# Kernel optimization log

Measured on AMD Instinct MI355X. Metric: run time of the kernel, lower is better.

## Reference

```python
import jax, jax.numpy as jnp
import numpy as np

B, S, D = 4, 4096, 1024
ROT = 4          # rotation_dim (quaternion)
MAX_SEQ = 4096   # max_seq_len
EPS = 1e-5


def setup_inputs() -> dict:
    key = jax.random.key(0)
    k_x, = jax.random.split(key, 1)
    x = jax.random.normal(k_x, (B, S, D), dtype=jnp.float32)
    # Learned parameters (torch inits: eye, ones, LN gamma=1 beta=0)
    rotation_matrix = jnp.eye(ROT, dtype=jnp.float32)
    frequency_kernel = jnp.ones((MAX_SEQ,), dtype=jnp.float32)
    ln_gamma = jnp.ones((D,), dtype=jnp.float32)
    ln_beta = jnp.zeros((D,), dtype=jnp.float32)
    return {"x": x, "rotation_matrix": rotation_matrix,
            "frequency_kernel": frequency_kernel,
            "ln_gamma": ln_gamma, "ln_beta": ln_beta}


def reference(x, rotation_matrix, frequency_kernel, ln_gamma, ln_beta):
    b, s, d = x.shape
    quat_dim = d // ROT
    # (b, s, quat_dim, 4)
    x_quat = x.reshape(b, s, quat_dim, ROT)
    # FFT along sequence axis, multiply by (real) learnable frequency kernel
    x_freq = jnp.fft.fft(x_quat, axis=1)
    kernel = frequency_kernel[:s].reshape(1, s, 1, 1)
    filtered_time = jnp.fft.ifft(x_freq * kernel, axis=1).real.astype(x.dtype)
    # Small 4x4 quaternion rotation applied to the last axis
    rotated = jnp.einsum('bstq,oq->bsto', filtered_time, rotation_matrix)
    out = rotated.reshape(b, s, d)
    # LayerNorm over the feature dim
    mean = jnp.mean(out, axis=-1, keepdims=True)
    var = jnp.var(out, axis=-1, keepdims=True)
    out = (out - mean) * jax.lax.rsqrt(var + EPS) * ln_gamma + ln_beta
    return out
```

## Files before the change

kernel.cpp:

```cpp
#include <hip/hip_runtime.h>
#include <hip/hip_bf16.h>

#define NB 4
#define NS 4096
#define ND 1024
#define NP 512
#define LN_EPS 1e-5f

__device__ __forceinline__ int pad(int i) { return i + (i >> 4); }

__device__ __forceinline__ float2 cadd(float2 a, float2 b) { return make_float2(a.x + b.x, a.y + b.y); }
__device__ __forceinline__ float2 csub(float2 a, float2 b) { return make_float2(a.x - b.x, a.y - b.y); }
__device__ __forceinline__ float2 cmul(float2 a, float2 b) {
  return make_float2(a.x * b.x - a.y * b.y, a.x * b.y + a.y * b.x);
}
__device__ __forceinline__ float2 cmulc(float2 a, float2 b) {
  return make_float2(a.x * b.x + a.y * b.y, a.y * b.x - a.x * b.y);
}
__device__ __forceinline__ unsigned short f2bf(float f) {
  unsigned int u = __float_as_uint(f);
  u += 0x7FFFu + ((u >> 16) & 1u);
  return (unsigned short)(u >> 16);
}
__device__ __forceinline__ float bf2f(unsigned int lo16) {
  return __uint_as_float(lo16 << 16);
}
__device__ __forceinline__ unsigned int packbf(float a, float b) {
  return (unsigned int)f2bf(a) | ((unsigned int)f2bf(b) << 16);
}

__device__ __forceinline__ int rev12(int p) {
  return ((p & 15) << 8) | (p & 240) | (p >> 8);
}

template<int S>
__device__ __forceinline__ void dft16(float2* x) {
  const float C1 = 0.9238795325112867f, S1 = 0.3826834323650898f, RT = 0.7071067811865476f;
  const float WC[10] = {1.f, C1, RT, S1, 0.f, -S1, -RT, -C1, -1.f, -C1};
  const float WS[10] = {0.f, S1, RT, C1, 1.f, C1,  RT,  S1,  0.f, -S1};
  #pragma unroll
  for (int m0 = 0; m0 < 4; ++m0) {
    float2 a = x[m0], b = x[m0 + 4], c = x[m0 + 8], d = x[m0 + 12];
    float2 t0 = cadd(a, c), t1 = csub(a, c), t2 = cadd(b, d), t3 = csub(b, d);
    float2 t3i = (S < 0) ? make_float2(t3.y, -t3.x) : make_float2(-t3.y, t3.x);
    x[m0]      = cadd(t0, t2);
    x[m0 + 4]  = cadd(t1, t3i);
    x[m0 + 8]  = csub(t0, t2);
    x[m0 + 12] = csub(t1, t3i);
  }
  #pragma unroll
  for (int r0 = 1; r0 < 4; ++r0)
    #pragma unroll
    for (int m0 = 1; m0 < 4; ++m0) {
      const int k = m0 * r0;
      const float2 w = make_float2(WC[k], (S < 0) ? -WS[k] : WS[k]);
      x[m0 + 4 * r0] = cmul(x[m0 + 4 * r0], w);
    }
  float2 y[16];
  #pragma unroll
  for (int r0 = 0; r0 < 4; ++r0) {
    float2 a = x[4 * r0], b = x[4 * r0 + 1], c = x[4 * r0 + 2], d = x[4 * r0 + 3];
    float2 t0 = cadd(a, c), t1 = csub(a, c), t2 = cadd(b, d), t3 = csub(b, d);
    float2 t3i = (S < 0) ? make_float2(t3.y, -t3.x) : make_float2(-t3.y, t3.x);
    y[r0]      = cadd(t0, t2);
    y[r0 + 4]  = cadd(t1, t3i);
    y[r0 + 8]  = csub(t0, t2);
    y[r0 + 12] = csub(t1, t3i);
  }
  #pragma unroll
  for (int i = 0; i < 16; ++i) x[i] = y[i];
}

__global__ void kprep(const float* __restrict__ fk, float* __restrict__ fkp,
                      float2* __restrict__ TwA, float2* __restrict__ TwC) {
  const int p = blockIdx.x * 256 + threadIdx.x;
  fkp[p] = fk[rev12(p)] * (1.0f / 4096.0f);
  const float TPON = 1.5339807878856412e-3f;
  if (p < 256) {
    const int a = p >> 4, r = p & 15;
    float sn, cs;
    __sincosf((float)(a * r) * (TPON * 16.f), &sn, &cs);
    TwA[p] = make_float2(cs, -sn);
    __sincosf((float)(a * r) * TPON, &sn, &cs);
    TwC[p] = make_float2(cs, -sn);
  }
}

__global__ __launch_bounds__(256) void ktransP(const float* __restrict__ x,
                                               unsigned int* __restrict__ xP) {
  __shared__ float tile[64][65];
  const int b = blockIdx.z;
  const int s0 = blockIdx.x * 64;
  const int d0 = blockIdx.y * 64;
  const int t = threadIdx.x;
  const float* xb = x + (size_t)b * NS * ND;
  #pragma unroll
  for (int p = 0; p < 4; ++p) {
    int r = (t >> 4) + p * 16;
    int c = (t & 15) * 4;
    float4 v = *reinterpret_cast<const float4*>(xb + (size_t)(s0 + r) * ND + (d0 + c));
    tile[r][c] = v.x; tile[r][c + 1] = v.y; tile[r][c + 2] = v.z; tile[r][c + 3] = v.w;
  }
  __syncthreads();
  const int pl = t >> 3;
  const int sc0 = (t & 7) * 8;
  unsigned int buf[8];
  #pragma unroll
  for (int j = 0; j < 8; ++j)
    buf[j] = packbf(tile[sc0 + j][2 * pl], tile[sc0 + j][2 * pl + 1]);
  unsigned int* dst = xP + (size_t)((b * NP) + (d0 >> 1) + pl) * NS + s0 + sc0;
  *reinterpret_cast<uint4*>(dst)     = make_uint4(buf[0], buf[1], buf[2], buf[3]);
  *reinterpret_cast<uint4*>(dst + 4) = make_uint4(buf[4], buf[5], buf[6], buf[7]);
}

__global__ __launch_bounds__(512, 4) void kfft(unsigned int* __restrict__ xP,
                                               const float* __restrict__ fkp,
                                               const float2* __restrict__ TwAg,
                                               const float2* __restrict__ TwCg,
                                               const float* __restrict__ R) {
  extern __shared__ unsigned char smem[];
  float2* zdyn = (float2*)smem;
  float2* twl = (float2*)(smem + 69632);
  const int t = threadIdx.x;
  const int h = t >> 8;
  const int tt = t & 255;
  const int q = blockIdx.x;
  const int b = blockIdx.y;
  const unsigned int* rowP = xP + (size_t)(b * NP + q * 2 + h) * NS;
  float2* zz = zdyn + (size_t)h * 4352;
  const int ta = tt >> 4, tc = tt & 15;
  float2 x[16];

  twl[t] = (t < 256) ? TwAg[t] : TwCg[t - 256];

  #pragma unroll
  for (int m = 0; m < 16; ++m) {
    unsigned int u = rowP[tt + 256 * m];
    x[m] = make_float2(bf2f(u & 0xffffu), bf2f(u >> 16));
  }
  dft16<-1>(x);
  __syncthreads();
  zz[pad(tt)] = x[0];
  #pragma unroll
  for (int r = 1; r < 16; ++r) {
    float2 tw = cmul(twl[r * 16 + ta], twl[256 + r * 16 + tc]);
    zz[pad(tt + 256 * r)] = cmul(x[r], tw);
  }
  __syncthreads();
  {
    const int bs = 256 * (tt >> 4) + (tt & 15);
    const int j = tt & 15;
    #pragma unroll
    for (int m = 0; m < 16; ++m) x[m] = zz[pad(bs + 16 * m)];
    dft16<-1>(x);
    zz[pad(bs)] = x[0];
    #pragma unroll
    for (int r = 1; r < 16; ++r) zz[pad(bs + 16 * r)] = cmul(x[r], twl[r * 16 + j]);
  }
  __syncthreads();
  {
    const int bs = 16 * tt;
    #pragma unroll
    for (int m = 0; m < 16; ++m) x[m] = zz[pad(bs + m)];
    dft16<-1>(x);
    #pragma unroll
    for (int r4 = 0; r4 < 4; ++r4) {
      float4 kv = *reinterpret_cast<const float4*>(fkp + bs + 4 * r4);
      x[4 * r4 + 0].x *= kv.x; x[4 * r4 + 0].y *= kv.x;
      x[4 * r4 + 1].x *= kv.y; x[4 * r4 + 1].y *= kv.y;
      x[4 * r4 + 2].x *= kv.z; x[4 * r4 + 2].y *= kv.z;
      x[4 * r4 + 3].x *= kv.w; x[4 * r4 + 3].y *= kv.w;
    }
    dft16<1>(x);
    #pragma unroll
    for (int r = 0; r < 16; ++r) zz[pad(bs + r)] = x[r];
  }
  __syncthreads();
  {
    const int bs = 256 * (tt >> 4) + (tt & 15);
    const int j = tt & 15;
    x[0] = zz[pad(bs)];
    #pragma unroll
    for (int m = 1; m < 16; ++m) x[m] = cmulc(zz[pad(bs + 16 * m)], twl[m * 16 + j]);
    dft16<1>(x);
    #pragma unroll
    for (int r = 0; r < 16; ++r) zz[pad(bs + 16 * r)] = x[r];
  }
  __syncthreads();
  {
    x[0] = zz[pad(tt)];
    #pragma unroll
    for (int m = 1; m < 16; ++m)
      x[m] = cmulc(cmulc(zz[pad(tt + 256 * m)], twl[m * 16 + ta]), twl[256 + m * 16 + tc]);
    dft16<1>(x);
    #pragma unroll
    for (int r = 0; r < 16; ++r) zz[pad(tt + 256 * r)] = x[r];
  }
  __syncthreads();
  const float r00 = R[0],  r01 = R[1],  r02 = R[2],  r03 = R[3];
  const float r10 = R[4],  r11 = R[5],  r12 = R[6],  r13 = R[7];
  const float r20 = R[8],  r21 = R[9],  r22 = R[10], r23 = R[11];
  const float r30 = R[12], r31 = R[13], r32 = R[14], r33 = R[15];
  unsigned int* row0 = xP + (size_t)(b * NP + q * 2) * NS;
  unsigned int* row1 = row0 + NS;
  #pragma unroll
  for (int k = 0; k < 8; ++k) {
    const int s = t + 512 * k;
    float2 v0 = zdyn[pad(s)];
    float2 v1 = zdyn[4352 + pad(s)];
    float c0 = v0.x, c1 = v0.y, c2 = v1.x, c3 = v1.y;
    float o0 = r00 * c0 + r01 * c1 + r02 * c2 + r03 * c3;
    float o1 = r10 * c0 + r11 * c1 + r12 * c2 + r13 * c3;
    float o2 = r20 * c0 + r21 * c1 + r22 * c2 + r23 * c3;
    float o3 = r30 * c0 + r31 * c1 + r32 * c2 + r33 * c3;
    row0[s] = packbf(o0, o1);
    row1[s] = packbf(o2, o3);
  }
}

__global__ __launch_bounds__(256) void kstatsP(const unsigned int* __restrict__ xP,
                                               float* __restrict__ ssum,
                                               float* __restrict__ ssq) {
  const int b = blockIdx.y;
  const int s0 = blockIdx.x * 64;
  const int w = threadIdx.x >> 6;
  const int l = threadIdx.x & 63;
  const unsigned int* src = xP + (size_t)b * NP * NS + s0 + l;
  float as = 0.f, aq = 0.f;
  for (int p = w * 4; p < NP; p += 16) {
    #pragma unroll
    for (int j = 0; j < 4; ++j) {
      unsigned int u = src[(size_t)(p + j) * NS];
      float v0 = bf2f(u & 0xffffu), v1 = bf2f(u >> 16);
      as += v0 + v1;
      aq += v0 * v0 + v1 * v1;
    }
  }
  __shared__ float rs[4][64], rq[4][64];
  rs[w][l] = as;
  rq[w][l] = aq;
  __syncthreads();
  if (w == 0) {
    ssum[b * NS + s0 + l] = (rs[0][l] + rs[1][l]) + (rs[2][l] + rs[3][l]);
    ssq[b * NS + s0 + l]  = (rq[0][l] + rq[1][l]) + (rq[2][l] + rq[3][l]);
  }
}

__global__ __launch_bounds__(256) void kapplyP(const unsigned int* __restrict__ xP,
                                               const float* __restrict__ ssum,
                                               const float* __restrict__ ssq,
                                               const float* __restrict__ gam,
                                               const float* __restrict__ bet,
                                               float* __restrict__ out) {
  __shared__ float tile[64][65];
  const int b = blockIdx.z;
  const int s0 = blockIdx.x * 64;
  const int d0 = blockIdx.y * 64;
  const int t = threadIdx.x;
  const int pl = t >> 3;
  const int sc0 = (t & 7) * 8;
  const unsigned int* src = xP + (size_t)(b * NP + (d0 >> 1) + pl) * NS + s0 + sc0;
  uint4 u0 = *reinterpret_cast<const uint4*>(src);
  uint4 u1 = *reinterpret_cast<const uint4*>(src + 4);
  const unsigned int uu[8] = {u0.x, u0.y, u0.z, u0.w, u1.x, u1.y, u1.z, u1.w};
  #pragma unroll
  for (int j = 0; j < 8; ++j) {
    tile[2 * pl][sc0 + j]     = bf2f(uu[j] & 0xffffu);
    tile[2 * pl + 1][sc0 + j] = bf2f(uu[j] >> 16);
  }
  __syncthreads();
  float* dst = out + ((size_t)b * NS + s0) * ND + d0;
  #pragma unroll
  for (int p = 0; p < 4; ++p) {
    int sr = (t >> 4) + p * 16;
    int s = s0 + sr;
    float mean = ssum[b * NS + s] * (1.0f / ND);
    float var = ssq[b * NS + s] * (1.0f / ND) - mean * mean;
    float inv = rsqrtf(var + LN_EPS);
    int dc = (t & 15) * 4;
    float4 g4 = *reinterpret_cast<const float4*>(gam + d0 + dc);
    float4 b4 = *reinterpret_cast<const float4*>(bet + d0 + dc);
    float4 o;
    o.x = (tile[dc + 0][sr] - mean) * inv * g4.x + b4.x;
    o.y = (tile[dc + 1][sr] - mean) * inv * g4.y + b4.y;
    o.z = (tile[dc + 2][sr] - mean) * inv * g4.z + b4.z;
    o.w = (tile[dc + 3][sr] - mean) * inv * g4.w + b4.w;
    *reinterpret_cast<float4*>(dst + (size_t)sr * ND + dc) = o;
  }
}

extern "C" void kernel_launch(void* const* d_in, const int* in_sizes, int n_in,
                              void* d_out, int out_size, void* d_ws, size_t ws_size,
                              hipStream_t stream) {
  const float* x  = (const float*)d_in[0];
  const float* R  = (const float*)d_in[1];
  const float* fk = (const float*)d_in[2];
  const float* gm = (const float*)d_in[3];
  const float* bt = (const float*)d_in[4];
  float* out = (float*)d_out;

  char* ws = (char*)d_ws;
  unsigned int* xP = (unsigned int*)ws;
  float*  ssum = (float*)(ws + (size_t)NB * NP * NS * 4);
  float*  ssq  = ssum + NB * NS;
  float*  fkp  = ssq + NB * NS;
  float2* TwA  = (float2*)(fkp + NS);
  float2* TwC  = TwA + 256;

  (void)hipFuncSetAttribute((const void*)kfft,
                            hipFuncAttributeMaxDynamicSharedMemorySize, 73728);

  kprep<<<16, 256, 0, stream>>>(fk, fkp, TwA, TwC);
  ktransP<<<dim3(NS / 64, ND / 64, NB), 256, 0, stream>>>(x, xP);
  kfft<<<dim3(ND / 4, NB), 512, 73728, stream>>>(xP, fkp, TwA, TwC, R);
  kstatsP<<<dim3(NS / 64, NB), 256, 0, stream>>>(xP, ssum, ssq);
  kapplyP<<<dim3(NS / 64, ND / 64, NB), 256, 0, stream>>>(xP, ssum, ssq, gm, bt, out);
}
```

Measured before the change: 93.81 us.

## Store FFT scratch as fp16 in LDS and fuse LayerNorm stats with apply

```diff
diff --git a/kernel.cpp b/kernel.cpp
--- a/kernel.cpp
+++ b/kernel.cpp
@@ -1,5 +1,6 @@
 #include <hip/hip_runtime.h>
 #include <hip/hip_bf16.h>
+#include <hip/hip_fp16.h>
 
 #define NB 4
 #define NS 4096
@@ -27,6 +28,14 @@
 }
 __device__ __forceinline__ unsigned int packbf(float a, float b) {
   return (unsigned int)f2bf(a) | ((unsigned int)f2bf(b) << 16);
+}
+__device__ __forceinline__ unsigned int pkh(float2 v) {
+  __half2 h = __floats2half2_rn(v.x, v.y);
+  return *reinterpret_cast<unsigned int*>(&h);
+}
+__device__ __forceinline__ float2 uph(unsigned int u) {
+  __half2 h = *reinterpret_cast<__half2*>(&u);
+  return __half22float2(h);
 }
 
 __device__ __forceinline__ int rev12(int p) {
@@ -119,15 +128,15 @@
                                                const float2* __restrict__ TwCg,
                                                const float* __restrict__ R) {
   extern __shared__ unsigned char smem[];
-  float2* zdyn = (float2*)smem;
-  float2* twl = (float2*)(smem + 69632);
+  unsigned int* zdyn = (unsigned int*)smem;
+  float2* twl = (float2*)(smem + 34816);
   const int t = threadIdx.x;
   const int h = t >> 8;
   const int tt = t & 255;
   const int q = blockIdx.x;
   const int b = blockIdx.y;
   const unsigned int* rowP = xP + (size_t)(b * NP + q * 2 + h) * NS;
-  float2* zz = zdyn + (size_t)h * 4352;
+  unsigned int* zz = zdyn + (size_t)h * 4352;
   const int ta = tt >> 4, tc = tt & 15;
   float2 x[16];
 
@@ -140,28 +149,28 @@
   }
   dft16<-1>(x);
   __syncthreads();
-  zz[pad(tt)] = x[0];
+  zz[pad(tt)] = pkh(x[0]);
   #pragma unroll
   for (int r = 1; r < 16; ++r) {
     float2 tw = cmul(twl[r * 16 + ta], twl[256 + r * 16 + tc]);
-    zz[pad(tt + 256 * r)] = cmul(x[r], tw);
+    zz[pad(tt + 256 * r)] = pkh(cmul(x[r], tw));
   }
   __syncthreads();
   {
     const int bs = 256 * (tt >> 4) + (tt & 15);
     const int j = tt & 15;
     #pragma unroll
-    for (int m = 0; m < 16; ++m) x[m] = zz[pad(bs + 16 * m)];
+    for (int m = 0; m < 16; ++m) x[m] = uph(zz[pad(bs + 16 * m)]);
     dft16<-1>(x);
-    zz[pad(bs)] = x[0];
-    #pragma unroll
-    for (int r = 1; r < 16; ++r) zz[pad(bs + 16 * r)] = cmul(x[r], twl[r * 16 + j]);
+    zz[pad(bs)] = pkh(x[0]);
+    #pragma unroll
+    for (int r = 1; r < 16; ++r) zz[pad(bs + 16 * r)] = pkh(cmul(x[r], twl[r * 16 + j]));
   }
   __syncthreads();
   {
     const int bs = 16 * tt;
     #pragma unroll
-    for (int m = 0; m < 16; ++m) x[m] = zz[pad(bs + m)];
+    for (int m = 0; m < 16; ++m) x[m] = uph(zz[pad(bs + m)]);
     dft16<-1>(x);
     #pragma unroll
     for (int r4 = 0; r4 < 4; ++r4) {
@@ -173,28 +182,28 @@
     }
     dft16<1>(x);
     #pragma unroll
-    for (int r = 0; r < 16; ++r) zz[pad(bs + r)] = x[r];
+    for (int r = 0; r < 16; ++r) zz[pad(bs + r)] = pkh(x[r]);
   }
   __syncthreads();
   {
     const int bs = 256 * (tt >> 4) + (tt & 15);
     const int j = tt & 15;
-    x[0] = zz[pad(bs)];
-    #pragma unroll
-    for (int m = 1; m < 16; ++m) x[m] = cmulc(zz[pad(bs + 16 * m)], twl[m * 16 + j]);
+    x[0] = uph(zz[pad(bs)]);
+    #pragma unroll
+    for (int m = 1; m < 16; ++m) x[m] = cmulc(uph(zz[pad(bs + 16 * m)]), twl[m * 16 + j]);
     dft16<1>(x);
     #pragma unroll
-    for (int r = 0; r < 16; ++r) zz[pad(bs + 16 * r)] = x[r];
+    for (int r = 0; r < 16; ++r) zz[pad(bs + 16 * r)] = pkh(x[r]);
   }
   __syncthreads();
   {
-    x[0] = zz[pad(tt)];
+    x[0] = uph(zz[pad(tt)]);
     #pragma unroll
     for (int m = 1; m < 16; ++m)
-      x[m] = cmulc(cmulc(zz[pad(tt + 256 * m)], twl[m * 16 + ta]), twl[256 + m * 16 + tc]);
+      x[m] = cmulc(cmulc(uph(zz[pad(tt + 256 * m)]), twl[m * 16 + ta]), twl[256 + m * 16 + tc]);
     dft16<1>(x);
     #pragma unroll
-    for (int r = 0; r < 16; ++r) zz[pad(tt + 256 * r)] = x[r];
+    for (int r = 0; r < 16; ++r) zz[pad(tt + 256 * r)] = pkh(x[r]);
   }
   __syncthreads();
   const float r00 = R[0],  r01 = R[1],  r02 = R[2],  r03 = R[3];
@@ -206,8 +215,8 @@
   #pragma unroll
   for (int k = 0; k < 8; ++k) {
     const int s = t + 512 * k;
-    float2 v0 = zdyn[pad(s)];
-    float2 v1 = zdyn[4352 + pad(s)];
+    float2 v0 = uph(zdyn[pad(s)]);
+    float2 v1 = uph(zdyn[4352 + pad(s)]);
     float c0 = v0.x, c1 = v0.y, c2 = v1.x, c3 = v1.y;
     float o0 = r00 * c0 + r01 * c1 + r02 * c2 + r03 * c3;
     float o1 = r10 * c0 + r11 * c1 + r12 * c2 + r13 * c3;
@@ -218,13 +227,18 @@
   }
 }
 
-__global__ __launch_bounds__(256) void kstatsP(const unsigned int* __restrict__ xP,
-                                               float* __restrict__ ssum,
-                                               float* __restrict__ ssq) {
+__global__ __launch_bounds__(256) void kapply2(const unsigned int* __restrict__ xP,
+                                               const float* __restrict__ gam,
+                                               const float* __restrict__ bet,
+                                               float* __restrict__ out) {
+  __shared__ float tile[64][65];
+  __shared__ float rs[4][64], rq[4][64];
+  __shared__ float smean[64], sinv[64];
   const int b = blockIdx.y;
   const int s0 = blockIdx.x * 64;
-  const int w = threadIdx.x >> 6;
-  const int l = threadIdx.x & 63;
+  const int t = threadIdx.x;
+  const int w = t >> 6;
+  const int l = t & 63;
   const unsigned int* src = xP + (size_t)b * NP * NS + s0 + l;
   float as = 0.f, aq = 0.f;
   for (int p = w * 4; p < NP; p += 16) {
@@ -236,56 +250,49 @@
       aq += v0 * v0 + v1 * v1;
     }
   }
-  __shared__ float rs[4][64], rq[4][64];
   rs[w][l] = as;
   rq[w][l] = aq;
   __syncthreads();
   if (w == 0) {
-    ssum[b * NS + s0 + l] = (rs[0][l] + rs[1][l]) + (rs[2][l] + rs[3][l]);
-    ssq[b * NS + s0 + l]  = (rq[0][l] + rq[1][l]) + (rq[2][l] + rq[3][l]);
-  }
-}
-
-__global__ __launch_bounds__(256) void kapplyP(const unsigned int* __restrict__ xP,
-                                               const float* __restrict__ ssum,
-                                               const float* __restrict__ ssq,
-                                               const float* __restrict__ gam,
-                                               const float* __restrict__ bet,
-                                               float* __restrict__ out) {
-  __shared__ float tile[64][65];
-  const int b = blockIdx.z;
-  const int s0 = blockIdx.x * 64;
-  const int d0 = blockIdx.y * 64;
-  const int t = threadIdx.x;
+    float sm = (rs[0][l] + rs[1][l]) + (rs[2][l] + rs[3][l]);
+    float sq = (rq[0][l] + rq[1][l]) + (rq[2][l] + rq[3][l]);
+    float mean = sm * (1.0f / ND);
+    float var = sq * (1.0f / ND) - mean * mean;
+    smean[l] = mean;
+    sinv[l] = rsqrtf(var + LN_EPS);
+  }
+  __syncthreads();
   const int pl = t >> 3;
   const int sc0 = (t & 7) * 8;
-  const unsigned int* src = xP + (size_t)(b * NP + (d0 >> 1) + pl) * NS + s0 + sc0;
-  uint4 u0 = *reinterpret_cast<const uint4*>(src);
-  uint4 u1 = *reinterpret_cast<const uint4*>(src + 4);
-  const unsigned int uu[8] = {u0.x, u0.y, u0.z, u0.w, u1.x, u1.y, u1.z, u1.w};
-  #pragma unroll
-  for (int j = 0; j < 8; ++j) {
-    tile[2 * pl][sc0 + j]     = bf2f(uu[j] & 0xffffu);
-    tile[2 * pl + 1][sc0 + j] = bf2f(uu[j] >> 16);
-  }
-  __syncthreads();
-  float* dst = out + ((size_t)b * NS + s0) * ND + d0;
-  #pragma unroll
-  for (int p = 0; p < 4; ++p) {
-    int sr = (t >> 4) + p * 16;
-    int s = s0 + sr;
-    float mean = ssum[b * NS + s] * (1.0f / ND);
-    float var = ssq[b * NS + s] * (1.0f / ND) - mean * mean;
-    float inv = rsqrtf(var + LN_EPS);
-    int dc = (t & 15) * 4;
-    float4 g4 = *reinterpret_cast<const float4*>(gam + d0 + dc);
-    float4 b4 = *reinterpret_cast<const float4*>(bet + d0 + dc);
-    float4 o;
-    o.x = (tile[dc + 0][sr] - mean) * inv * g4.x + b4.x;
-    o.y = (tile[dc + 1][sr] - mean) * inv * g4.y + b4.y;
-    o.z = (tile[dc + 2][sr] - mean) * inv * g4.z + b4.z;
-    o.w = (tile[dc + 3][sr] - mean) * inv * g4.w + b4.w;
-    *reinterpret_cast<float4*>(dst + (size_t)sr * ND + dc) = o;
+  for (int c = 0; c < ND / 64; ++c) {
+    const int d0 = c * 64;
+    const unsigned int* srcc = xP + (size_t)(b * NP + (d0 >> 1) + pl) * NS + s0 + sc0;
+    uint4 u0 = *reinterpret_cast<const uint4*>(srcc);
+    uint4 u1 = *reinterpret_cast<const uint4*>(srcc + 4);
+    const unsigned int uu[8] = {u0.x, u0.y, u0.z, u0.w, u1.x, u1.y, u1.z, u1.w};
+    #pragma unroll
+    for (int j = 0; j < 8; ++j) {
+      tile[2 * pl][sc0 + j]     = bf2f(uu[j] & 0xffffu);
+      tile[2 * pl + 1][sc0 + j] = bf2f(uu[j] >> 16);
+    }
+    __syncthreads();
+    float* dst = out + ((size_t)b * NS + s0) * ND + d0;
+    #pragma unroll
+    for (int p = 0; p < 4; ++p) {
+      int sr = (t >> 4) + p * 16;
+      float mean = smean[sr];
+      float inv = sinv[sr];
+      int dc = (t & 15) * 4;
+      float4 g4 = *reinterpret_cast<const float4*>(gam + d0 + dc);
+      float4 b4 = *reinterpret_cast<const float4*>(bet + d0 + dc);
+      float4 o;
+      o.x = (tile[dc + 0][sr] - mean) * inv * g4.x + b4.x;
+      o.y = (tile[dc + 1][sr] - mean) * inv * g4.y + b4.y;
+      o.z = (tile[dc + 2][sr] - mean) * inv * g4.z + b4.z;
+      o.w = (tile[dc + 3][sr] - mean) * inv * g4.w + b4.w;
+      *reinterpret_cast<float4*>(dst + (size_t)sr * ND + dc) = o;
+    }
+    __syncthreads();
   }
 }
 
@@ -301,18 +308,15 @@
 
   char* ws = (char*)d_ws;
   unsigned int* xP = (unsigned int*)ws;
-  float*  ssum = (float*)(ws + (size_t)NB * NP * NS * 4);
-  float*  ssq  = ssum + NB * NS;
-  float*  fkp  = ssq + NB * NS;
+  float*  fkp  = (float*)(ws + (size_t)NB * NP * NS * 4);
   float2* TwA  = (float2*)(fkp + NS);
   float2* TwC  = TwA + 256;
 
   (void)hipFuncSetAttribute((const void*)kfft,
-                            hipFuncAttributeMaxDynamicSharedMemorySize, 73728);
+                            hipFuncAttributeMaxDynamicSharedMemorySize, 38912);
 
   kprep<<<16, 256, 0, stream>>>(fk, fkp, TwA, TwC);
   ktransP<<<dim3(NS / 64, ND / 64, NB), 256, 0, stream>>>(x, xP);
-  kfft<<<dim3(ND / 4, NB), 512, 73728, stream>>>(xP, fkp, TwA, TwC, R);
-  kstatsP<<<dim3(NS / 64, NB), 256, 0, stream>>>(xP, ssum, ssq);
-  kapplyP<<<dim3(NS / 64, ND / 64, NB), 256, 0, stream>>>(xP, ssum, ssq, gm, bt, out);
-}
+  kfft<<<dim3(ND / 4, NB), 512, 38912, stream>>>(xP, fkp, TwA, TwC, R);
+  kapply2<<<dim3(NS / 64, NB), 256, 0, stream>>>(xP, gm, bt, out);
+}
```

Result: no change. 95.36 us (+1.7%).
